# Kernel tuning notes

Hardware: AMD Instinct MI355X
Metric: run time of the kernel (lower is better)

## Reference

```python
import jax, jax.numpy as jnp
import numpy as np

B_GRAPHS = 64      # number of graphs in the batch
NODES_PER_G = 1600 # nodes per graph (equal-size for simplicity; math is ragged-safe via segment_sum)
N = B_GRAPHS * NODES_PER_G  # 102400 nodes
F_DIM = 128
K_CLUSTERS = 16
AVG_DEG = 32
E = N * AVG_DEG  # 3276800 edges


def setup_inputs() -> dict:
    key = jax.random.key(0)
    k1, k2, k3, k4, k5, k6 = jax.random.split(key, 6)
    x = jax.random.normal(k1, (N, F_DIM), jnp.float32)
    W = jax.random.normal(k2, (F_DIM, K_CLUSTERS), jnp.float32) * (1.0 / np.sqrt(F_DIM))
    b = jnp.zeros((K_CLUSTERS,), jnp.float32)
    # edges are constrained to lie within a graph (adjacency is block-diagonal across graphs)
    g = jax.random.randint(k3, (E,), 0, B_GRAPHS)
    edge_src = jax.random.randint(k4, (E,), 0, NODES_PER_G) + g * NODES_PER_G
    edge_dst = jax.random.randint(k5, (E,), 0, NODES_PER_G) + g * NODES_PER_G
    edge_weight = jax.random.uniform(k6, (E,), jnp.float32)
    batch = jnp.repeat(jnp.arange(B_GRAPHS), NODES_PER_G)  # sorted graph ids, as batch2ptr requires
    return {"x": x, "W": W, "b": b, "edge_weight": edge_weight,
            "edge_src": edge_src, "edge_dst": edge_dst, "batch": batch}


def reference(x, W, b, edge_weight, edge_src, edge_dst, batch):
    K = W.shape[1]
    Bn = B_GRAPHS
    n_nodes = x.shape[0]
    # forward() applies softmax once, then mincut_pool applies softmax again (temp=1.0)
    s = jax.nn.softmax(x @ W + b, axis=-1)
    s = jax.nn.softmax(s, axis=-1)                      # [N, K]
    # d = adj.sum(axis=0): column sums of the sparse adjacency
    deg = jax.ops.segment_sum(edge_weight, edge_dst, num_segments=n_nodes)  # [N]
    # M = A @ S without materializing block-diagonal C_bd:  M[i] = sum_j w_ij * s[j]
    M = jax.ops.segment_sum(edge_weight[:, None] * s[edge_dst], edge_src, num_segments=n_nodes)  # [N, K]
    # out_adj blocks: S_b^T A_b S_b  -> [B, K, K]  (C_bd^T A C_bd is block-diagonal)
    out_adj = jax.ops.segment_sum(s[:, :, None] * M[:, None, :], batch, num_segments=Bn)
    # mincut loss = -trace(C^T A C) / trace(C^T D C)
    mincut_num = jnp.sum(jnp.trace(out_adj, axis1=1, axis2=2))
    mincut_den = jnp.sum(deg * jnp.sum(s * s, axis=1))
    mincut_loss = -mincut_num / mincut_den
    # CC blocks: S_b^T S_b -> [B, K, K]
    CC = jax.ops.segment_sum(s[:, :, None] * s[:, None, :], batch, num_segments=Bn)
    cc_norm = jnp.sqrt(jnp.sum(CC * CC, axis=(1, 2)))   # per-graph Frobenius norm of CC block
    eye_div_k = jnp.eye(K, dtype=x.dtype) / jnp.sqrt(jnp.asarray(K, x.dtype))
    diff = CC / cc_norm[:, None, None] - eye_div_k
    ortho_loss = jnp.mean(jnp.sqrt(jnp.sum(diff * diff, axis=(1, 2))))
    # mask diagonal of pooled adjacency, then symmetric degree-normalize
    out_adj = out_adj * (1.0 - jnp.eye(K, dtype=x.dtype))
    d_pool = jnp.sqrt(jnp.sum(out_adj, axis=2)) + 1e-12  # [B, K] row sums -> sqrt + eps
    out_adj_n = out_adj / (d_pool[:, :, None] * d_pool[:, None, :])
    # out_x: per-graph S_b^T X_b, vstacked -> [B*K, F]; module applies SELU
    out_x = jax.ops.segment_sum(s[:, :, None] * x[:, None, :], batch, num_segments=Bn)
    out_x = jax.nn.selu(out_x.reshape(Bn * K, -1))
    return out_x, out_adj_n, mincut_loss, ortho_loss
```

## Files before the change

### kernel.cpp

```cpp
#include <hip/hip_runtime.h>
#include <math.h>

#define NN 102400
#define FD 128
#define KC 16
#define BG 64
#define NPG 1600
#define NE 3276800
#define HB 640
#define EH (NE / HB)
#define EPT (EH / 256)
#define BINS 256
#define RPB 400
#define NPB 160

__device__ __forceinline__ void glob_addf(float* p, float v) {
  unsafeAtomicAdd(p, v);
}
__device__ __forceinline__ unsigned f2bf(float f) {
  unsigned u = __float_as_uint(f);
  u += 0x7FFFu + ((u >> 16) & 1u);
  return (u >> 16) & 0xFFFFu;
}
__device__ __forceinline__ float bf2f(unsigned h) {
  return __uint_as_float(h << 16);
}

__global__ __launch_bounds__(256, 4) void k_s2(const float* __restrict__ x,
    const float* __restrict__ W, const float* __restrict__ bb,
    const int* __restrict__ esrc, float* __restrict__ s,
    unsigned short* __restrict__ blkhist, float* __restrict__ cc_part,
    float* __restrict__ outx_part) {
  __shared__ float st[NPB * KC];
  __shared__ unsigned h[BINS];
  const int t = threadIdx.x, b = blockIdx.x;
  const int g = b / 10, sub = b % 10;
  const int n0 = g * NPG + sub * NPB;
  h[t] = 0u;
  __syncthreads();
  const int e0 = b * EH;
  for (int i = t; i < EH; i += 256) {
    unsigned bin = (unsigned)esrc[e0 + i] / (unsigned)RPB;
    atomicAdd(&h[bin], 1u);
  }
  __syncthreads();
  blkhist[t * HB + b] = (unsigned short)h[t];
  if (t < NPB) {
    float acc[KC];
#pragma unroll
    for (int k = 0; k < KC; ++k) acc[k] = bb[k];
    const float4* xr = (const float4*)(x + (size_t)(n0 + t) * FD);
#pragma unroll 4
    for (int c = 0; c < FD / 4; ++c) {
      float4 v = xr[c];
      const float* wr = W + c * 4 * KC;
#pragma unroll
      for (int k = 0; k < KC; ++k)
        acc[k] += v.x * wr[k] + v.y * wr[KC + k] + v.z * wr[2 * KC + k] + v.w * wr[3 * KC + k];
    }
#pragma unroll
    for (int r = 0; r < 2; ++r) {
      float m = acc[0];
#pragma unroll
      for (int k = 1; k < KC; ++k) m = fmaxf(m, acc[k]);
      float sum = 0.f;
#pragma unroll
      for (int k = 0; k < KC; ++k) { acc[k] = expf(acc[k] - m); sum += acc[k]; }
      float inv = 1.f / sum;
#pragma unroll
      for (int k = 0; k < KC; ++k) acc[k] *= inv;
    }
#pragma unroll
    for (int k = 0; k < KC; ++k) st[t * KC + k] = acc[k];
    float4* so = (float4*)(s + (size_t)(n0 + t) * KC);
    so[0] = make_float4(acc[0], acc[1], acc[2], acc[3]);
    so[1] = make_float4(acc[4], acc[5], acc[6], acc[7]);
    so[2] = make_float4(acc[8], acc[9], acc[10], acc[11]);
    so[3] = make_float4(acc[12], acc[13], acc[14], acc[15]);
  }
  __syncthreads();
  const int j = t & 127, h2 = t >> 7;
  const int kc = t >> 4, lc = t & 15;
  float accX[8] = {0.f, 0.f, 0.f, 0.f, 0.f, 0.f, 0.f, 0.f};
  float accC = 0.f;
  for (int i = 0; i < NPB; ++i) {
    const float xv = x[(size_t)(n0 + i) * FD + j];
    const float* si = st + i * KC;
#pragma unroll
    for (int kk = 0; kk < 8; ++kk) accX[kk] = fmaf(si[h2 * 8 + kk], xv, accX[kk]);
    accC = fmaf(si[kc], si[lc], accC);
  }
#pragma unroll
  for (int kk = 0; kk < 8; ++kk)
    outx_part[(size_t)b * 2048 + (h2 * 8 + kk) * 128 + j] = accX[kk];
  cc_part[b * 256 + t] = accC;
}

__global__ __launch_bounds__(640) void k_scan_a(unsigned short* __restrict__ blkhist,
    unsigned* __restrict__ gtot, unsigned* __restrict__ azero) {
  __shared__ unsigned wsum[10];
  const int t = threadIdx.x, bin = blockIdx.x;
  const int lane = t & 63;
  const unsigned zi = (unsigned)bin * 640u + (unsigned)t;
  if (zi < 16400u) azero[zi] = 0u;
  unsigned v = blkhist[bin * HB + t];
  unsigned inc = v;
#pragma unroll
  for (int o = 1; o < 64; o <<= 1) {
    unsigned nb = __shfl_up(inc, o, 64);
    if (lane >= o) inc += nb;
  }
  if (lane == 63) wsum[t >> 6] = inc;
  __syncthreads();
  if (t == 0) {
    unsigned run = 0;
#pragma unroll
    for (int i = 0; i < 10; ++i) { unsigned c = wsum[i]; wsum[i] = run; run += c; }
    gtot[bin] = run;
  }
  __syncthreads();
  blkhist[bin * HB + t] = (unsigned short)(inc - v + wsum[t >> 6]);
}

__global__ __launch_bounds__(256, 4) void k_scatter2(const float* __restrict__ ew,
    const int* __restrict__ esrc, const int* __restrict__ edst,
    const unsigned short* __restrict__ blkhist, const unsigned* __restrict__ gtot,
    unsigned short* __restrict__ skey, unsigned* __restrict__ pay) {
  __shared__ unsigned cur[BINS];
  __shared__ unsigned gadj[BINS];
  __shared__ unsigned wsum[4];
  __shared__ unsigned pays[EH];
  __shared__ unsigned short keys[EH];
  __shared__ unsigned char bmap[EH];
  const int t = threadIdx.x, b = blockIdx.x;
  const unsigned gv = gtot[t];
  unsigned ginc = gv;
#pragma unroll
  for (int o = 1; o < 64; o <<= 1) {
    unsigned nb = __shfl_up(ginc, o, 64);
    if ((t & 63) >= o) ginc += nb;
  }
  if ((t & 63) == 63) wsum[t >> 6] = ginc;
  __syncthreads();
  if (t == 0) {
    unsigned run = 0;
#pragma unroll
    for (int i = 0; i < 4; ++i) { unsigned c = wsum[i]; wsum[i] = run; run += c; }
  }
  __syncthreads();
  const unsigned gstart = (ginc - gv + wsum[t >> 6]) + blkhist[t * HB + b];
  cur[t] = 0u;
  __syncthreads();
  unsigned rpay[EPT], rmeta[EPT];
  const int e0 = b * EH;
#pragma unroll
  for (int i = 0; i < EPT; ++i) {
    const int e = e0 + t + i * 256;
    int s0 = esrc[e], d0 = edst[e];
    float w = ew[e];
    unsigned bin = (unsigned)s0 / (unsigned)RPB;
    unsigned g = bin >> 2;
    rmeta[i] = (bin << 16) | ((unsigned)s0 - bin * RPB);
    rpay[i] = (((unsigned)d0 - g * NPG) << 16) | f2bf(w);
    atomicAdd(&cur[bin], 1u);
  }
  __syncthreads();
  {
    unsigned v = cur[t];
    unsigned inc = v;
#pragma unroll
    for (int o = 1; o < 64; o <<= 1) {
      unsigned nb = __shfl_up(inc, o, 64);
      if ((t & 63) >= o) inc += nb;
    }
    if ((t & 63) == 63) wsum[t >> 6] = inc;
    __syncthreads();
    if (t == 0) {
      unsigned run = 0;
#pragma unroll
      for (int i = 0; i < 4; ++i) { unsigned c = wsum[i]; wsum[i] = run; run += c; }
    }
    __syncthreads();
    const unsigned boff = inc - v + wsum[t >> 6];
    cur[t] = boff;
    gadj[t] = gstart - boff;
  }
  __syncthreads();
#pragma unroll
  for (int i = 0; i < EPT; ++i) {
    const unsigned bin = rmeta[i] >> 16;
    const unsigned pos = atomicAdd(&cur[bin], 1u);
    pays[pos] = rpay[i];
    keys[pos] = (unsigned short)(rmeta[i] & 0xFFFFu);
    bmap[pos] = (unsigned char)bin;
  }
  __syncthreads();
  for (int p = t; p < EH; p += 256) {
    const unsigned bin = bmap[p];
    const unsigned ga = gadj[bin] + p;
    pay[ga] = pays[p];
    skey[ga] = keys[p];
  }
}

__global__ __launch_bounds__(1024, 1) void k_msc3(const float* __restrict__ s,
    const unsigned short* __restrict__ skey, const unsigned* __restrict__ pay,
    const unsigned* __restrict__ gtot, float* __restrict__ adj_raw,
    float* __restrict__ den) {
  __shared__ float SL[NPG * 17];
  __shared__ unsigned Ml[RPB * 17];
  __shared__ float P[1024];
  __shared__ float scr[16];
  __shared__ unsigned gbl[257];
  const int t = threadIdx.x;
  const int bin = (blockIdx.x & 7) * 32 + (blockIdx.x >> 3);
  const int g = bin >> 2;
  const int q = bin & 3;
  if (t < 64) {
    unsigned v0 = gtot[t * 4], v1 = gtot[t * 4 + 1];
    unsigned v2 = gtot[t * 4 + 2], v3 = gtot[t * 4 + 3];
    unsigned sum = v0 + v1 + v2 + v3;
    unsigned inc = sum;
#pragma unroll
    for (int o = 1; o < 64; o <<= 1) {
      unsigned nb = __shfl_up(inc, o, 64);
      if (t >= o) inc += nb;
    }
    unsigned ex = inc - sum;
    gbl[t * 4] = ex;
    gbl[t * 4 + 1] = ex + v0;
    gbl[t * 4 + 2] = ex + v0 + v1;
    gbl[t * 4 + 3] = ex + v0 + v1 + v2;
    if (t == 63) gbl[256] = inc;
  }
  const float4* sg4 = (const float4*)(s + (size_t)g * NPG * KC);
  for (int u4 = t; u4 < NPG * KC / 4; u4 += 1024) {
    float4 v = sg4[u4];
    const int u = u4 * 4;
    float* d = &SL[(u >> 4) * 17 + (u & 15)];
    d[0] = v.x; d[1] = v.y; d[2] = v.z; d[3] = v.w;
  }
  for (int i = t; i < RPB * 17; i += 1024) Ml[i] = 0u;
  __syncthreads();
  const unsigned gb = gbl[bin], ge = gbl[bin + 1];
  const int l = t & 15;
  const int gid = t >> 4;
  const float FXS = 16777216.f;
  float dacc = 0.f;
  unsigned e = gb + gid;
  for (; e + 448 < ge; e += 512) {
    unsigned pk0 = pay[e],       pk1 = pay[e + 64];
    unsigned pk2 = pay[e + 128], pk3 = pay[e + 192];
    unsigned pk4 = pay[e + 256], pk5 = pay[e + 320];
    unsigned pk6 = pay[e + 384], pk7 = pay[e + 448];
    unsigned sk0 = skey[e],       sk1 = skey[e + 64];
    unsigned sk2 = skey[e + 128], sk3 = skey[e + 192];
    unsigned sk4 = skey[e + 256], sk5 = skey[e + 320];
    unsigned sk6 = skey[e + 384], sk7 = skey[e + 448];
    float sv0 = SL[(pk0 >> 16) * 17 + l];
    float sv1 = SL[(pk1 >> 16) * 17 + l];
    float sv2 = SL[(pk2 >> 16) * 17 + l];
    float sv3 = SL[(pk3 >> 16) * 17 + l];
    float sv4 = SL[(pk4 >> 16) * 17 + l];
    float sv5 = SL[(pk5 >> 16) * 17 + l];
    float sv6 = SL[(pk6 >> 16) * 17 + l];
    float sv7 = SL[(pk7 >> 16) * 17 + l];
    float t0 = bf2f(pk0 & 0xFFFFu) * sv0;
    float t1 = bf2f(pk1 & 0xFFFFu) * sv1;
    float t2 = bf2f(pk2 & 0xFFFFu) * sv2;
    float t3 = bf2f(pk3 & 0xFFFFu) * sv3;
    float t4 = bf2f(pk4 & 0xFFFFu) * sv4;
    float t5 = bf2f(pk5 & 0xFFFFu) * sv5;
    float t6 = bf2f(pk6 & 0xFFFFu) * sv6;
    float t7 = bf2f(pk7 & 0xFFFFu) * sv7;
    dacc = fmaf(t0, sv0, dacc);
    dacc = fmaf(t1, sv1, dacc);
    dacc = fmaf(t2, sv2, dacc);
    dacc = fmaf(t3, sv3, dacc);
    dacc = fmaf(t4, sv4, dacc);
    dacc = fmaf(t5, sv5, dacc);
    dacc = fmaf(t6, sv6, dacc);
    dacc = fmaf(t7, sv7, dacc);
    atomicAdd(&Ml[sk0 * 17 + l], __float2uint_rn(t0 * FXS));
    atomicAdd(&Ml[sk1 * 17 + l], __float2uint_rn(t1 * FXS));
    atomicAdd(&Ml[sk2 * 17 + l], __float2uint_rn(t2 * FXS));
    atomicAdd(&Ml[sk3 * 17 + l], __float2uint_rn(t3 * FXS));
    atomicAdd(&Ml[sk4 * 17 + l], __float2uint_rn(t4 * FXS));
    atomicAdd(&Ml[sk5 * 17 + l], __float2uint_rn(t5 * FXS));
    atomicAdd(&Ml[sk6 * 17 + l], __float2uint_rn(t6 * FXS));
    atomicAdd(&Ml[sk7 * 17 + l], __float2uint_rn(t7 * FXS));
  }
  for (; e < ge; e += 64) {
    unsigned pk0 = pay[e];
    unsigned sk0 = skey[e];
    float sv0 = SL[(pk0 >> 16) * 17 + l];
    float t0 = bf2f(pk0 & 0xFFFFu) * sv0;
    dacc = fmaf(t0, sv0, dacc);
    atomicAdd(&Ml[sk0 * 17 + l], __float2uint_rn(t0 * FXS));
  }
  __syncthreads();
  const int ck = (t >> 4) & 15, cl = t & 15, sub = t >> 8;
  float pacc = 0.f;
  const float* SLq = SL + q * RPB * 17;
#pragma unroll 4
  for (int ii = 0; ii < RPB / 4; ++ii) {
    const int r = sub + 4 * ii;
    pacc = fmaf(SLq[r * 17 + ck], (float)Ml[r * 17 + cl], pacc);
  }
  P[t] = pacc;
#pragma unroll
  for (int o = 32; o > 0; o >>= 1) dacc += __shfl_down(dacc, o, 64);
  if ((t & 63) == 0) scr[t >> 6] = dacc;
  __syncthreads();
  if (t < 256) glob_addf(adj_raw + g * 256 + t,
                         (P[t] + P[t + 256] + P[t + 512] + P[t + 768])
                             * 5.9604644775390625e-8f);
  if (t == 0) {
    float sum = 0.f;
#pragma unroll
    for (int i = 0; i < 16; ++i) sum += scr[i];
    glob_addf(den, sum);
  }
}

__device__ __forceinline__ float bred(float v, float* scr) {
#pragma unroll
  for (int o = 32; o > 0; o >>= 1) v += __shfl_down(v, o, 64);
  __syncthreads();
  if ((threadIdx.x & 63) == 0) scr[threadIdx.x >> 6] = v;
  __syncthreads();
  return scr[0] + scr[1] + scr[2] + scr[3];
}

__global__ __launch_bounds__(256) void k_post(const float* __restrict__ adj_raw,
    const float* __restrict__ cc_part, const float* __restrict__ outx_part,
    float* __restrict__ out, float* __restrict__ scal, unsigned* __restrict__ done) {
  const int b = blockIdx.x, t = threadIdx.x;
  const int k = t >> 4, l = t & 15;
  __shared__ float m[16 * 17];
  __shared__ float dk[16];
  __shared__ float scr[4];
  const float raw = adj_raw[b * 256 + t];
  const float masked = (k == l) ? 0.f : raw;
  m[k * 17 + l] = masked;
  __syncthreads();
  if (t < 16) {
    float rs = 0.f;
#pragma unroll
    for (int ll = 0; ll < 16; ++ll) rs += m[t * 17 + ll];
    dk[t] = sqrtf(rs) + 1e-12f;
  }
  __syncthreads();
  out[131072 + b * 256 + t] = masked / (dk[k] * dk[l]);
  float tr = bred((k == l) ? raw : 0.f, scr);
  if (t == 0) glob_addf(scal + 1, tr);
  float c = 0.f;
#pragma unroll
  for (int u = 0; u < 10; ++u) c += cc_part[(b * 10 + u) * 256 + t];
  float n2 = bred(c * c, scr);
  float diff = c / sqrtf(n2) - ((k == l) ? 0.25f : 0.f);
  float d2 = bred(diff * diff, scr);
  if (t == 0) glob_addf(scal + 2, sqrtf(d2));
  for (int idx = b * 256 + t; idx < 131072; idx += 16384) {
    const int gg = idx >> 11, v = idx & 2047;
    float xv = 0.f;
#pragma unroll
    for (int u = 0; u < 10; ++u) xv += outx_part[(size_t)(gg * 10 + u) * 2048 + v];
    out[idx] = xv > 0.f ? 1.0507009873554805f * xv
                        : 1.0507009873554805f * 1.6732632423543772f * expm1f(xv);
  }
  __syncthreads();
  if (t == 0) {
    __threadfence();
    unsigned v = __hip_atomic_fetch_add(done, 1u, __ATOMIC_ACQ_REL,
                                        __HIP_MEMORY_SCOPE_AGENT);
    if (v == 63u) {
      float den   = __hip_atomic_load(scal + 0, __ATOMIC_RELAXED, __HIP_MEMORY_SCOPE_AGENT);
      float num   = __hip_atomic_load(scal + 1, __ATOMIC_RELAXED, __HIP_MEMORY_SCOPE_AGENT);
      float ortho = __hip_atomic_load(scal + 2, __ATOMIC_RELAXED, __HIP_MEMORY_SCOPE_AGENT);
      out[147456] = -num / den;
      out[147457] = ortho * (1.f / 64.f);
    }
  }
}

extern "C" void kernel_launch(void* const* d_in, const int* in_sizes, int n_in,
                              void* d_out, int out_size, void* d_ws, size_t ws_size,
                              hipStream_t stream) {
  const float* x  = (const float*)d_in[0];
  const float* W  = (const float*)d_in[1];
  const float* bb = (const float*)d_in[2];
  const float* ew = (const float*)d_in[3];
  const int* esrc = (const int*)d_in[4];
  const int* edst = (const int*)d_in[5];
  float* out = (float*)d_out;
  float* ws = (float*)d_ws;

  float* s_buf    = ws;
  float* adj_raw  = s_buf + (size_t)NN * KC;
  float* scal     = adj_raw + 16384;
  unsigned* done  = (unsigned*)(scal + 8);
  float* cc_part  = (float*)(done + 8);
  float* outx_part= cc_part + (size_t)HB * 256;
  unsigned* gtot  = (unsigned*)(outx_part + (size_t)HB * 2048);
  unsigned short* blkhist = (unsigned short*)(gtot + BINS);
  unsigned short* skey = blkhist + (size_t)BINS * HB;
  unsigned* pay = (unsigned*)(skey + NE);

  k_s2<<<HB, 256, 0, stream>>>(x, W, bb, esrc, s_buf, blkhist, cc_part, outx_part);
  k_scan_a<<<BINS, 640, 0, stream>>>(blkhist, gtot, (unsigned*)adj_raw);
  k_scatter2<<<HB, 256, 0, stream>>>(ew, esrc, edst, blkhist, gtot, skey, pay);
  k_msc3<<<BINS, 1024, 0, stream>>>(s_buf, skey, pay, gtot, adj_raw, scal);
  k_post<<<64, 256, 0, stream>>>(adj_raw, cc_part, outx_part, out, scal, done);
}
```

Before: 214.8 us.

## Replace histogram+scan bucketing with fixed-capacity bins and atomic cursors

After: 213.1 us. About the same (-0.8%).

```diff
diff --git a/kernel.cpp b/kernel.cpp
--- a/kernel.cpp
+++ b/kernel.cpp
@@ -12,7 +12,9 @@
 #define EPT (EH / 256)
 #define BINS 256
 #define RPB 400
-#define NPB 160
+#define CAP 13824
+#define NPB 200
+#define SB 512
 
 __device__ __forceinline__ void glob_addf(float* p, float v) {
   unsafeAtomicAdd(p, v);
@@ -28,23 +30,18 @@
 
 __global__ __launch_bounds__(256, 4) void k_s2(const float* __restrict__ x,
     const float* __restrict__ W, const float* __restrict__ bb,
-    const int* __restrict__ esrc, float* __restrict__ s,
-    unsigned short* __restrict__ blkhist, float* __restrict__ cc_part,
-    float* __restrict__ outx_part) {
+    float* __restrict__ s, float* __restrict__ cc_part,
+    float* __restrict__ outx_part, unsigned* __restrict__ azero,
+    unsigned* __restrict__ gcur) {
   __shared__ float st[NPB * KC];
-  __shared__ unsigned h[BINS];
   const int t = threadIdx.x, b = blockIdx.x;
-  const int g = b / 10, sub = b % 10;
+  const int g = b >> 3, sub = b & 7;
   const int n0 = g * NPG + sub * NPB;
-  h[t] = 0u;
-  __syncthreads();
-  const int e0 = b * EH;
-  for (int i = t; i < EH; i += 256) {
-    unsigned bin = (unsigned)esrc[e0 + i] / (unsigned)RPB;
-    atomicAdd(&h[bin], 1u);
-  }
-  __syncthreads();
-  blkhist[t * HB + b] = (unsigned short)h[t];
+  {
+    const unsigned gid = (unsigned)b * 256u + (unsigned)t;
+    if (gid < 16400u) azero[gid] = 0u;
+    else if (gid < 16656u) gcur[gid - 16400u] = (gid - 16400u) * CAP;
+  }
   if (t < NPB) {
     float acc[KC];
 #pragma unroll
@@ -96,35 +93,9 @@
   cc_part[b * 256 + t] = accC;
 }
 
-__global__ __launch_bounds__(640) void k_scan_a(unsigned short* __restrict__ blkhist,
-    unsigned* __restrict__ gtot, unsigned* __restrict__ azero) {
-  __shared__ unsigned wsum[10];
-  const int t = threadIdx.x, bin = blockIdx.x;
-  const int lane = t & 63;
-  const unsigned zi = (unsigned)bin * 640u + (unsigned)t;
-  if (zi < 16400u) azero[zi] = 0u;
-  unsigned v = blkhist[bin * HB + t];
-  unsigned inc = v;
-#pragma unroll
-  for (int o = 1; o < 64; o <<= 1) {
-    unsigned nb = __shfl_up(inc, o, 64);
-    if (lane >= o) inc += nb;
-  }
-  if (lane == 63) wsum[t >> 6] = inc;
-  __syncthreads();
-  if (t == 0) {
-    unsigned run = 0;
-#pragma unroll
-    for (int i = 0; i < 10; ++i) { unsigned c = wsum[i]; wsum[i] = run; run += c; }
-    gtot[bin] = run;
-  }
-  __syncthreads();
-  blkhist[bin * HB + t] = (unsigned short)(inc - v + wsum[t >> 6]);
-}
-
 __global__ __launch_bounds__(256, 4) void k_scatter2(const float* __restrict__ ew,
     const int* __restrict__ esrc, const int* __restrict__ edst,
-    const unsigned short* __restrict__ blkhist, const unsigned* __restrict__ gtot,
+    unsigned* __restrict__ gcur,
     unsigned short* __restrict__ skey, unsigned* __restrict__ pay) {
   __shared__ unsigned cur[BINS];
   __shared__ unsigned gadj[BINS];
@@ -133,22 +104,6 @@
   __shared__ unsigned short keys[EH];
   __shared__ unsigned char bmap[EH];
   const int t = threadIdx.x, b = blockIdx.x;
-  const unsigned gv = gtot[t];
-  unsigned ginc = gv;
-#pragma unroll
-  for (int o = 1; o < 64; o <<= 1) {
-    unsigned nb = __shfl_up(ginc, o, 64);
-    if ((t & 63) >= o) ginc += nb;
-  }
-  if ((t & 63) == 63) wsum[t >> 6] = ginc;
-  __syncthreads();
-  if (t == 0) {
-    unsigned run = 0;
-#pragma unroll
-    for (int i = 0; i < 4; ++i) { unsigned c = wsum[i]; wsum[i] = run; run += c; }
-  }
-  __syncthreads();
-  const unsigned gstart = (ginc - gv + wsum[t >> 6]) + blkhist[t * HB + b];
   cur[t] = 0u;
   __syncthreads();
   unsigned rpay[EPT], rmeta[EPT];
@@ -182,6 +137,7 @@
     }
     __syncthreads();
     const unsigned boff = inc - v + wsum[t >> 6];
+    const unsigned gstart = atomicAdd(&gcur[t], v);
     cur[t] = boff;
     gadj[t] = gstart - boff;
   }
@@ -205,34 +161,16 @@
 
 __global__ __launch_bounds__(1024, 1) void k_msc3(const float* __restrict__ s,
     const unsigned short* __restrict__ skey, const unsigned* __restrict__ pay,
-    const unsigned* __restrict__ gtot, float* __restrict__ adj_raw,
+    const unsigned* __restrict__ gcur, float* __restrict__ adj_raw,
     float* __restrict__ den) {
   __shared__ float SL[NPG * 17];
   __shared__ unsigned Ml[RPB * 17];
   __shared__ float P[1024];
   __shared__ float scr[16];
-  __shared__ unsigned gbl[257];
   const int t = threadIdx.x;
   const int bin = (blockIdx.x & 7) * 32 + (blockIdx.x >> 3);
   const int g = bin >> 2;
   const int q = bin & 3;
-  if (t < 64) {
-    unsigned v0 = gtot[t * 4], v1 = gtot[t * 4 + 1];
-    unsigned v2 = gtot[t * 4 + 2], v3 = gtot[t * 4 + 3];
-    unsigned sum = v0 + v1 + v2 + v3;
-    unsigned inc = sum;
-#pragma unroll
-    for (int o = 1; o < 64; o <<= 1) {
-      unsigned nb = __shfl_up(inc, o, 64);
-      if (t >= o) inc += nb;
-    }
-    unsigned ex = inc - sum;
-    gbl[t * 4] = ex;
-    gbl[t * 4 + 1] = ex + v0;
-    gbl[t * 4 + 2] = ex + v0 + v1;
-    gbl[t * 4 + 3] = ex + v0 + v1 + v2;
-    if (t == 63) gbl[256] = inc;
-  }
   const float4* sg4 = (const float4*)(s + (size_t)g * NPG * KC);
   for (int u4 = t; u4 < NPG * KC / 4; u4 += 1024) {
     float4 v = sg4[u4];
@@ -242,7 +180,7 @@
   }
   for (int i = t; i < RPB * 17; i += 1024) Ml[i] = 0u;
   __syncthreads();
-  const unsigned gb = gbl[bin], ge = gbl[bin + 1];
+  const unsigned gb = (unsigned)bin * CAP, ge = gcur[bin];
   const int l = t & 15;
   const int gid = t >> 4;
   const float FXS = 16777216.f;
@@ -356,7 +294,7 @@
   if (t == 0) glob_addf(scal + 1, tr);
   float c = 0.f;
 #pragma unroll
-  for (int u = 0; u < 10; ++u) c += cc_part[(b * 10 + u) * 256 + t];
+  for (int u = 0; u < 8; ++u) c += cc_part[(b * 8 + u) * 256 + t];
   float n2 = bred(c * c, scr);
   float diff = c / sqrtf(n2) - ((k == l) ? 0.25f : 0.f);
   float d2 = bred(diff * diff, scr);
@@ -365,7 +303,7 @@
     const int gg = idx >> 11, v = idx & 2047;
     float xv = 0.f;
 #pragma unroll
-    for (int u = 0; u < 10; ++u) xv += outx_part[(size_t)(gg * 10 + u) * 2048 + v];
+    for (int u = 0; u < 8; ++u) xv += outx_part[(size_t)(gg * 8 + u) * 2048 + v];
     out[idx] = xv > 0.f ? 1.0507009873554805f * xv
                         : 1.0507009873554805f * 1.6732632423543772f * expm1f(xv);
   }
@@ -401,15 +339,14 @@
   float* scal     = adj_raw + 16384;
   unsigned* done  = (unsigned*)(scal + 8);
   float* cc_part  = (float*)(done + 8);
-  float* outx_part= cc_part + (size_t)HB * 256;
-  unsigned* gtot  = (unsigned*)(outx_part + (size_t)HB * 2048);
-  unsigned short* blkhist = (unsigned short*)(gtot + BINS);
-  unsigned short* skey = blkhist + (size_t)BINS * HB;
-  unsigned* pay = (unsigned*)(skey + NE);
-
-  k_s2<<<HB, 256, 0, stream>>>(x, W, bb, esrc, s_buf, blkhist, cc_part, outx_part);
-  k_scan_a<<<BINS, 640, 0, stream>>>(blkhist, gtot, (unsigned*)adj_raw);
-  k_scatter2<<<HB, 256, 0, stream>>>(ew, esrc, edst, blkhist, gtot, skey, pay);
-  k_msc3<<<BINS, 1024, 0, stream>>>(s_buf, skey, pay, gtot, adj_raw, scal);
+  float* outx_part= cc_part + (size_t)SB * 256;
+  unsigned* gcur  = (unsigned*)(outx_part + (size_t)SB * 2048);
+  unsigned short* skey = (unsigned short*)(gcur + BINS);
+  unsigned* pay = (unsigned*)(skey + (size_t)BINS * CAP);
+
+  k_s2<<<SB, 256, 0, stream>>>(x, W, bb, s_buf, cc_part, outx_part,
+                               (unsigned*)adj_raw, gcur);
+  k_scatter2<<<HB, 256, 0, stream>>>(ew, esrc, edst, gcur, skey, pay);
+  k_msc3<<<BINS, 1024, 0, stream>>>(s_buf, skey, pay, gcur, adj_raw, scal);
   k_post<<<64, 256, 0, stream>>>(adj_raw, cc_part, outx_part, out, scal, done);
 }
```
